# Performance work log

Hardware: AMD Instinct MI355X
Metric: run time of the kernel (lower is better)

Reference implementation:

```python
import jax, jax.numpy as jnp
import numpy as np
from jax import lax


def _cdist(a, b):
    # a: [B,N,D], b: [B,M,D] -> [B,N,M] euclidean distances (torch.cdist p=2)
    d2 = (jnp.sum(a * a, -1)[:, :, None]
          + jnp.sum(b * b, -1)[:, None, :]
          - 2.0 * jnp.einsum('bnd,bmd->bnm', a, b))
    return jnp.sqrt(jnp.maximum(d2, 0.0))


def _conv(x, w, b, pad):
    # x: [N,C,H,W], w: [O,I,kh,kw]
    y = lax.conv_general_dilated(x, w, (1, 1), [(pad, pad), (pad, pad)],
                                 dimension_numbers=('NCHW', 'OIHW', 'NCHW'))
    return y + b[None, :, None, None]


def setup_inputs() -> dict:
    key = jax.random.key(0)
    ks = jax.random.split(key, 10)
    Tq, Tk, D = 2048, 2048, 512
    return dict(
        seq_q=jax.random.normal(ks[0], (1, Tq, D), jnp.float32),
        seq_k=jax.random.normal(ks[1], (1, Tk, D), jnp.float32),
        len_q=jax.random.uniform(ks[2], (1, Tq), dtype=jnp.float32),
        len_k=jax.random.uniform(ks[3], (1, Tk), dtype=jnp.float32),
        conv1_w=jax.random.normal(ks[4], (30, 2, 5, 5), jnp.float32) * 0.1,
        conv1_b=jnp.zeros((30,), jnp.float32),
        conv2_w=jax.random.normal(ks[5], (30, 30, 5, 5), jnp.float32) * 0.05,
        conv2_b=jnp.zeros((30,), jnp.float32),
        conv3_w=jax.random.normal(ks[6], (1, 30, 3, 3), jnp.float32) * 0.1,
        conv3_b=jnp.zeros((1,), jnp.float32),
    )


def reference(seq_q, seq_k, len_q, len_k,
              conv1_w, conv1_b, conv2_w, conv2_b, conv3_w, conv3_b):
    B, Tq, _ = seq_q.shape
    Tk = seq_k.shape[1]
    D = _cdist(seq_q, seq_k)                          # [1,Tq,Tk]
    P = _cdist(len_q[..., None], len_k[..., None])    # [1,Tq,Tk]
    A = jnp.concatenate([D, P], 0)[None]              # [1,2,Tq,Tk]
    A = jax.nn.relu(_conv(A, conv1_w, conv1_b, 2))    # [1,30,Tq,Tk]
    A = jax.nn.relu(_conv(A, conv2_w, conv2_b, 2))    # [1,30,Tq,Tk]
    A = _conv(A, conv3_w, conv3_b, 1)[:, 0] + D       # [1,Tq,Tk] residual
    A = jax.nn.softmax(-A, axis=2)                    # row softmax
    At = A.reshape(B, Tq * Tk, 1)
    At = At / jnp.sum(jnp.abs(At), axis=1, keepdims=True)  # global L1 norm
    dis = jnp.matmul(D.reshape(B, 1, Tq * Tk), At)    # [1,1,1]
    return A, dis
```

## Files before the change

kernel.cpp:

```cpp
#include <hip/hip_runtime.h>

typedef short s8v __attribute__((ext_vector_type(8)));
typedef float f4v __attribute__((ext_vector_type(4)));

__device__ __forceinline__ unsigned short f2bf(float x) {
  union { float f; unsigned u; } v; v.f = x;
  unsigned r = v.u + 0x7fffu + ((v.u >> 16) & 1u);
  return (unsigned short)(r >> 16);
}
__device__ __forceinline__ unsigned pack_bf16x2(float lo, float hi) {
  unsigned r;
  asm("v_cvt_pk_bf16_f32 %0, %1, %2" : "=v"(r) : "v"(lo), "v"(hi));
  return r;
}
__device__ __forceinline__ s8v as_s8(int4 v) { union { int4 i; s8v s; } u; u.i = v; return u.s; }
__device__ __forceinline__ f4v as_f4(int4 v) { union { int4 i; f4v f; } u; u.i = v; return u.f; }
__device__ __forceinline__ int4 as_i4(f4v v) { union { f4v f; int4 i; } u; u.f = v; return u.i; }

__device__ __forceinline__ void bar_lgkm() {
  asm volatile("s_waitcnt lgkmcnt(0)" ::: "memory");
  __builtin_amdgcn_s_barrier();
  asm volatile("" ::: "memory");
}

__global__ __launch_bounds__(256) void prep_kernel(
    const float* __restrict__ q, const float* __restrict__ k,
    const float* __restrict__ w1, const float* __restrict__ w2, const float* __restrict__ w3,
    unsigned short* __restrict__ Qb, unsigned short* __restrict__ Kb,
    unsigned short* __restrict__ W1, unsigned short* __restrict__ W2,
    unsigned short* __restrict__ W3, float* __restrict__ nq, float* __restrict__ nk,
    float* __restrict__ accum) {
  int idx = blockIdx.x * 256 + threadIdx.x;
  const int NQ4 = (2048 * 512) / 4;
  if (idx < NQ4) {
    float4 v = ((const float4*)q)[idx];
    ((uint2*)Qb)[idx] = make_uint2(pack_bf16x2(v.x, v.y), pack_bf16x2(v.z, v.w));
    return;
  }
  idx -= NQ4;
  if (idx < NQ4) {
    float4 v = ((const float4*)k)[idx];
    ((uint2*)Kb)[idx] = make_uint2(pack_bf16x2(v.x, v.y), pack_bf16x2(v.z, v.w));
    return;
  }
  idx -= NQ4;
  if (idx < 4096 * 64) {
    int row = idx >> 6, l = idx & 63;
    const float* src = (row < 2048) ? (q + row * 512) : (k + (row - 2048) * 512);
    float s = 0.f;
#pragma unroll
    for (int i = 0; i < 8; ++i) { float v = src[l + i * 64]; s += v * v; }
    for (int off = 32; off; off >>= 1) s += __shfl_xor(s, off);
    if (l == 0) { if (row < 2048) nq[row] = s; else nk[row - 2048] = s; }
    return;
  }
  idx -= 4096 * 64;
  if (idx < 3072) {
    int j = idx >> 10, m = (idx >> 5) & 31, kk = idx & 31;
    int half = kk >> 4, kl = kk & 15, dy = 2 * j + half;
    float v = 0.f;
    if (m < 30 && kl < 10 && dy < 5) v = w1[m * 50 + (kl & 1) * 25 + dy * 5 + (kl >> 1)];
    W1[idx] = f2bf(v); return;
  }
  idx -= 3072;
  if (idx < 25600) {
    int dy = idx / 5120, r = idx - dy * 5120, m = r / 160, kk = r - m * 160;
    int c = kk & 31, dx = kk >> 5;
    float v = 0.f;
    if (m < 30 && c < 30) v = w2[m * 750 + c * 25 + dy * 5 + dx];
    W2[idx] = f2bf(v); return;
  }
  idx -= 25600;
  if (idx < 288) {
    int dd = idx >> 5, c = idx & 31;
    float v = (c < 30) ? w3[c * 9 + dd] : 0.f;
    W3[idx] = f2bf(v); return;
  }
  idx -= 288;
  if (idx == 0) *accum = 0.f;
}

__global__ __launch_bounds__(256) void dgemm_kernel(
    const unsigned short* __restrict__ Qb, const unsigned short* __restrict__ Kb,
    const float* __restrict__ nq, const float* __restrict__ nk,
    const float* __restrict__ lq, const float* __restrict__ lk,
    float* __restrict__ Dout, unsigned* __restrict__ DPo) {
  __shared__ int4 sm[2 * 128 * 9];
  const int t = threadIdx.x;
  const int bm = blockIdx.x, bn = blockIdx.y;
  const int wv = t >> 6, l = t & 63;
  const int m0 = (wv & 1) * 64, n0 = (wv >> 1) * 64;
  const int l15 = l & 15, q4 = l >> 4;
  f4v acc[4][4] = {};
  const int4* Qg = (const int4*)Qb;
  const int4* Kg = (const int4*)Kb;
  for (int kt = 0; kt < 8; ++kt) {
    __syncthreads();
#pragma unroll
    for (int i = 0; i < 4; ++i) {
      int c = t + i * 256;
      int row = c >> 3, kq = c & 7;
      sm[row * 9 + kq]        = Qg[(bm * 128 + row) * 64 + kt * 8 + kq];
      sm[1152 + row * 9 + kq] = Kg[(bn * 128 + row) * 64 + kt * 8 + kq];
    }
    __syncthreads();
#pragma unroll
    for (int s = 0; s < 2; ++s) {
      s8v af[4], bfr[4];
#pragma unroll
      for (int mt = 0; mt < 4; ++mt)
        af[mt] = as_s8(sm[(m0 + mt * 16 + l15) * 9 + s * 4 + q4]);
#pragma unroll
      for (int nt = 0; nt < 4; ++nt)
        bfr[nt] = as_s8(sm[1152 + (n0 + nt * 16 + l15) * 9 + s * 4 + q4]);
#pragma unroll
      for (int mt = 0; mt < 4; ++mt)
#pragma unroll
        for (int nt = 0; nt < 4; ++nt)
          acc[mt][nt] = __builtin_amdgcn_mfma_f32_16x16x32_bf16(af[mt], bfr[nt], acc[mt][nt], 0, 0, 0);
    }
  }
  float nkv[4], lkv[4];
#pragma unroll
  for (int nt = 0; nt < 4; ++nt) {
    int gc = bn * 128 + n0 + nt * 16 + l15;
    nkv[nt] = nk[gc]; lkv[nt] = lk[gc];
  }
#pragma unroll
  for (int mt = 0; mt < 4; ++mt)
#pragma unroll
    for (int reg = 0; reg < 4; ++reg) {
      int gr = bm * 128 + m0 + mt * 16 + q4 * 4 + reg;
      float nqv = nq[gr], lqv = lq[gr];
#pragma unroll
      for (int nt = 0; nt < 4; ++nt) {
        int gc = bn * 128 + n0 + nt * 16 + l15;
        float d2 = nqv + nkv[nt] - 2.f * acc[mt][nt][reg];
        float Dv = sqrtf(fmaxf(d2, 0.f));
        Dout[gr * 2048 + gc] = Dv;
        float Pv = fabsf(lqv - lkv[nt]);
        DPo[gr * 2048 + gc] = pack_bf16x2(Dv, Pv);
      }
    }
}

__global__ __launch_bounds__(512, 2) void fused_conv(
    const unsigned* __restrict__ DPg, const float* __restrict__ Dmat,
    const unsigned short* __restrict__ W1g, const unsigned short* __restrict__ W2g,
    const unsigned short* __restrict__ W3g,
    const float* __restrict__ b1, const float* __restrict__ b2, const float* __restrict__ b3,
    float* __restrict__ Sout) {
  __shared__ int4 a1s[1600];
  __shared__ int4 a2s[1360];
  __shared__ unsigned dps[1700];
  const int t = threadIdx.x;
  const int wv = t >> 6, l = t & 63, l15 = l & 15, q4 = l >> 4;
  const int x0 = blockIdx.x * 62, y0 = blockIdx.y * 32;

  int4 uni[25];
  int4 uni2[5];
  int4 ring2[5];
  float bias4[4];
  const int cls = (wv < 4) ? 0 : (wv < 6 ? 1 : 2);
  const int mb = (cls == 0) ? (wv >> 1) : (wv & 1);
  const int tp = (wv & 1) * 2;
  const int T3 = (wv - 6) * 2;

  unsigned pvO0 = 0u, pvO1 = 0u;
  float d0Oa = 0.f, d1Oa = 0.f, d0Ob = 0.f, d1Ob = 0.f;
  const int spx = (wv == 6) ? l : (64 + l);
  const int sgx = x0 - 5 + spx;
  const bool scol = (spx < 96) && (sgx >= 0) && (sgx < 2048);
  const int sgxc = min(max(sgx, 0), 2047);

  if (cls == 0) {
    const int4* W2i = (const int4*)W2g;
#pragma unroll
    for (int d = 0; d < 5; ++d)
#pragma unroll
      for (int s = 0; s < 5; ++s)
        uni[d * 5 + s] = W2i[(d * 32 + mb * 16 + l15) * 20 + s * 4 + q4];
#pragma unroll
    for (int j = 0; j < 5; ++j) { uni2[j] = make_int4(0, 0, 0, 0); ring2[j] = make_int4(0, 0, 0, 0); }
#pragma unroll
    for (int i = 0; i < 4; ++i) {
      int ch = mb * 16 + q4 * 4 + i;
      bias4[i] = (ch < 30) ? b2[ch] : 0.f;
    }
  } else if (cls == 1) {
    const int4* W1i = (const int4*)W1g;
#pragma unroll
    for (int j = 0; j < 3; ++j) uni2[j] = W1i[(j * 32 + mb * 16 + l15) * 4 + q4];
#pragma unroll
    for (int i = 0; i < 4; ++i) {
      int ch = mb * 16 + q4 * 4 + i;
      bias4[i] = (ch < 30) ? b1[ch] : 0.f;
    }
  } else {
    const int4* W3i = (const int4*)W3g;
#pragma unroll
    for (int dx = 0; dx < 3; ++dx)
      uni2[dx] = (l15 < 3) ? W3i[(l15 * 3 + dx) * 4 + q4] : make_int4(0, 0, 0, 0);
#pragma unroll
    for (int j = 0; j < 6; ++j) uni[j] = make_int4(0, 0, 0, 0);
    bias4[0] = b3[0];
    if (scol) {
      pvO0 = DPg[(y0 + 1) * 2048 + sgx];
      pvO1 = DPg[(y0 + 2) * 2048 + sgx];
    }
  }
  {
    int row = y0 - 5 + t / 96, px = t % 96;
    int gx = x0 - 5 + px;
    unsigned v = 0u;
    if (row >= 0 && gx >= 0 && gx < 2048) v = DPg[row * 2048 + gx];
    dps[(row & 15) * 100 + px] = v;
  }
  {
    int t2 = t + 512;
    if (t2 < 576) {
      int row = y0 - 5 + t2 / 96, px = t2 % 96;
      int gx = x0 - 5 + px;
      unsigned v = 0u;
      if (row >= 0 && gx >= 0 && gx < 2048) v = DPg[row * 2048 + gx];
      dps[(row & 15) * 100 + px] = v;
    }
  }
  if (t >= 144 && t < 224) {
    int i = t - 144;
    int sl = i >> 4, rem = i & 15;
    a2s[(sl * 68 + 64 + (rem >> 2)) * 4 + (rem & 3)] = make_int4(0, 0, 0, 0);
  }
  __syncthreads();

  for (int r = y0 - 3; r <= y0 + 37; r += 2) {
    if (cls == 0) {
#pragma unroll
      for (int sub = 0; sub < 2; ++sub) {
        int rc = r - 2 + sub;
        int s4 = rc & 3;
        int px0A = tp * 16 + l15;
        int px0B = px0A + 16;
        s8v fa = as_s8(a1s[(s4 * 80 + px0A) * 4 + (q4 ^ ((px0A >> 1) & 3))]);
        s8v fb = as_s8(a1s[(s4 * 80 + px0B) * 4 + (q4 ^ ((px0B >> 1) & 3))]);
        __builtin_amdgcn_s_setprio(1);
#pragma unroll
        for (int s = 0; s < 5; ++s) {
          s8v na = fa, nb = fb;
          if (s < 4) {
            int pxA = tp * 16 + l15 + s + 1;
            int pxB = pxA + 16;
            na = as_s8(a1s[(s4 * 80 + pxA) * 4 + (q4 ^ ((pxA >> 1) & 3))]);
            nb = as_s8(a1s[(s4 * 80 + pxB) * 4 + (q4 ^ ((pxB >> 1) & 3))]);
          }
#pragma unroll
          for (int d = 4; d >= 0; --d)
            uni2[4 - d] = as_i4(__builtin_amdgcn_mfma_f32_16x16x32_bf16(
                as_s8(uni[d * 5 + s]), fa, as_f4(uni2[4 - d]), 0, 0, 0));
#pragma unroll
          for (int d = 4; d >= 0; --d)
            ring2[4 - d] = as_i4(__builtin_amdgcn_mfma_f32_16x16x32_bf16(
                as_s8(uni[d * 5 + s]), fb, as_f4(ring2[4 - d]), 0, 0, 0));
          fa = na; fb = nb;
        }
        __builtin_amdgcn_s_setprio(0);
        int r2c = rc - 2;
        bool vrow = (r2c >= y0 - 1 && r2c <= y0 + 32);
        int slotrow = vrow ? (r2c & 3) : 4;
        bool rowin = vrow && (r2c >= 0) && (r2c < 2048);
        {
          int px2 = tp * 16 + l15;
          int gx2 = x0 - 1 + px2;
          bool ok = rowin && (gx2 >= 0) && (gx2 < 2048);
          f4v a = as_f4(uni2[0]);
          float v0 = ok ? fmaxf(a[0] + bias4[0], 0.f) : 0.f;
          float v1 = ok ? fmaxf(a[1] + bias4[1], 0.f) : 0.f;
          float v2 = ok ? fmaxf(a[2] + bias4[2], 0.f) : 0.f;
          float v3 = ok ? fmaxf(a[3] + bias4[3], 0.f) : 0.f;
          int slot = (mb * 2 + (q4 >> 1)) ^ ((px2 >> 1) & 3);
          *(uint2*)((unsigned short*)a2s + (slotrow * 68 + px2) * 32 + slot * 8 + (q4 & 1) * 4) =
              make_uint2(pack_bf16x2(v0, v1), pack_bf16x2(v2, v3));
        }
        {
          int px2 = tp * 16 + 16 + l15;
          int gx2 = x0 - 1 + px2;
          bool ok = rowin && (gx2 >= 0) && (gx2 < 2048);
          f4v a = as_f4(ring2[0]);
          float v0 = ok ? fmaxf(a[0] + bias4[0], 0.f) : 0.f;
          float v1 = ok ? fmaxf(a[1] + bias4[1], 0.f) : 0.f;
          float v2 = ok ? fmaxf(a[2] + bias4[2], 0.f) : 0.f;
          float v3 = ok ? fmaxf(a[3] + bias4[3], 0.f) : 0.f;
          int slot = (mb * 2 + (q4 >> 1)) ^ ((px2 >> 1) & 3);
          *(uint2*)((unsigned short*)a2s + (slotrow * 68 + px2) * 32 + slot * 8 + (q4 & 1) * 4) =
              make_uint2(pack_bf16x2(v0, v1), pack_bf16x2(v2, v3));
        }
#pragma unroll
        for (int j = 0; j < 4; ++j) { uni2[j] = uni2[j + 1]; ring2[j] = ring2[j + 1]; }
        uni2[4] = make_int4(0, 0, 0, 0);
        ring2[4] = make_int4(0, 0, 0, 0);
      }
    } else if (cls == 1) {
#pragma unroll
      for (int pr = 0; pr < 2; ++pr) {
        int p = r + pr;
        f4v a5[5];
        int4 c0, c1, c2;
        {
          int px = l15;
          int rl0 = p - 2, rl1 = p, rl2 = p + 2;
          int rs0 = (q4 < 2) ? rl0 : (rl0 + 1);
          int rs1 = (q4 < 2) ? rl1 : (rl1 + 1);
          c0 = *(const int4*)(dps + (rs0 & 15) * 100 + px + (q4 & 1) * 4);
          c1 = *(const int4*)(dps + (rs1 & 15) * 100 + px + (q4 & 1) * 4);
          c2 = *(const int4*)(dps + (rl2 & 15) * 100 + px + (q4 & 1) * 4);
        }
        __builtin_amdgcn_s_setprio(1);
#pragma unroll
        for (int T1 = 0; T1 < 5; ++T1) {
          int4 n0 = c0, n1 = c1, n2 = c2;
          if (T1 < 4) {
            int px = (T1 + 1) * 16 + l15;
            int rl0 = p - 2, rl1 = p, rl2 = p + 2;
            int rs0 = (q4 < 2) ? rl0 : (rl0 + 1);
            int rs1 = (q4 < 2) ? rl1 : (rl1 + 1);
            n0 = *(const int4*)(dps + (rs0 & 15) * 100 + px + (q4 & 1) * 4);
            n1 = *(const int4*)(dps + (rs1 & 15) * 100 + px + (q4 & 1) * 4);
            n2 = *(const int4*)(dps + (rl2 & 15) * 100 + px + (q4 & 1) * 4);
          }
          f4v acc = {0.f, 0.f, 0.f, 0.f};
          acc = __builtin_amdgcn_mfma_f32_16x16x32_bf16(as_s8(uni2[0]), as_s8(c0), acc, 0, 0, 0);
          acc = __builtin_amdgcn_mfma_f32_16x16x32_bf16(as_s8(uni2[1]), as_s8(c1), acc, 0, 0, 0);
          acc = __builtin_amdgcn_mfma_f32_16x16x32_bf16(as_s8(uni2[2]), as_s8(c2), acc, 0, 0, 0);
          a5[T1] = acc;
          c0 = n0; c1 = n1; c2 = n2;
        }
        __builtin_amdgcn_s_setprio(0);
        bool vrow = (p >= y0 - 3 && p <= y0 + 34);
        int slotrow = vrow ? (p & 3) : 4;
        bool rowok = vrow && (p >= 0 && p < 2048);
#pragma unroll
        for (int T1 = 0; T1 < 5; ++T1) {
          int px = T1 * 16 + l15;
          int gx = x0 - 3 + px;
          bool ok = rowok && gx >= 0 && gx < 2048;
          float v0 = ok ? fmaxf(a5[T1][0] + bias4[0], 0.f) : 0.f;
          float v1 = ok ? fmaxf(a5[T1][1] + bias4[1], 0.f) : 0.f;
          float v2 = ok ? fmaxf(a5[T1][2] + bias4[2], 0.f) : 0.f;
          float v3 = ok ? fmaxf(a5[T1][3] + bias4[3], 0.f) : 0.f;
          int slot = (mb * 2 + (q4 >> 1)) ^ ((px >> 1) & 3);
          *(uint2*)((unsigned short*)a1s + (slotrow * 80 + px) * 32 + slot * 8 + (q4 & 1) * 4) =
              make_uint2(pack_bf16x2(v0, v1), pack_bf16x2(v2, v3));
        }
      }
    } else {
      int rsN0 = r + 6, rsN1 = r + 7;
      unsigned tmp0 = DPg[min(rsN0, 2047) * 2048 + sgxc];
      unsigned tmp1 = DPg[min(rsN1, 2047) * 2048 + sgxc];
      unsigned pvN0 = (scol && rsN0 < 2048) ? tmp0 : 0u;
      unsigned pvN1 = (scol && rsN1 < 2048) ? tmp1 : 0u;
      int gx0 = x0 + T3 * 16 + l15;
      int gx0c = min(gx0, 2047), gx1c = min(gx0 + 16, 2047);
      int yn0c = min(max(r - 5, 0), 2047), yn1c = min(max(r - 4, 0), 2047);
      float d0Na = Dmat[yn0c * 2048 + gx0c];
      float d1Na = Dmat[yn0c * 2048 + gx1c];
      float d0Nb = Dmat[yn1c * 2048 + gx0c];
      float d1Nb = Dmat[yn1c * 2048 + gx1c];
      s8v Bf[12];
#pragma unroll
      for (int sub = 0; sub < 2; ++sub) {
        int s4 = (r - 6 + sub) & 3;
#pragma unroll
        for (int tt = 0; tt < 2; ++tt)
#pragma unroll
          for (int dx = 0; dx < 3; ++dx) {
            int px2 = (T3 + tt) * 16 + l15 + dx;
            Bf[sub * 6 + tt * 3 + dx] =
                as_s8(a2s[(s4 * 68 + px2) * 4 + (q4 ^ ((px2 >> 1) & 3))]);
          }
      }
      float eA0, eA1, eA2, eA3, eA4, eA5;
      {
        __builtin_amdgcn_s_setprio(1);
#pragma unroll
        for (int tt = 0; tt < 2; ++tt) {
          f4v acc3 = {0.f, 0.f, 0.f, 0.f};
#pragma unroll
          for (int dx = 0; dx < 3; ++dx)
            acc3 = __builtin_amdgcn_mfma_f32_16x16x32_bf16(
                as_s8(uni2[dx]), Bf[tt * 3 + dx], acc3, 0, 0, 0);
          uni[tt * 3 + 2] = as_i4(acc3);
        }
        __builtin_amdgcn_s_setprio(0);
        eA0 = as_f4(uni[0])[0]; eA1 = as_f4(uni[1])[1]; eA2 = as_f4(uni[2])[2];
        eA3 = as_f4(uni[3])[0]; eA4 = as_f4(uni[4])[1]; eA5 = as_f4(uni[5])[2];
#pragma unroll
        for (int tt = 0; tt < 2; ++tt) {
          uni[tt * 3 + 0] = uni[tt * 3 + 1];
          uni[tt * 3 + 1] = uni[tt * 3 + 2];
        }
      }
      float eB0, eB1, eB2, eB3, eB4, eB5;
      {
        __builtin_amdgcn_s_setprio(1);
#pragma unroll
        for (int tt = 0; tt < 2; ++tt) {
          f4v acc3 = {0.f, 0.f, 0.f, 0.f};
#pragma unroll
          for (int dx = 0; dx < 3; ++dx)
            acc3 = __builtin_amdgcn_mfma_f32_16x16x32_bf16(
                as_s8(uni2[dx]), Bf[6 + tt * 3 + dx], acc3, 0, 0, 0);
          uni[tt * 3 + 2] = as_i4(acc3);
        }
        __builtin_amdgcn_s_setprio(0);
        eB0 = as_f4(uni[0])[0]; eB1 = as_f4(uni[1])[1]; eB2 = as_f4(uni[2])[2];
        eB3 = as_f4(uni[3])[0]; eB4 = as_f4(uni[4])[1]; eB5 = as_f4(uni[5])[2];
#pragma unroll
        for (int tt = 0; tt < 2; ++tt) {
          uni[tt * 3 + 0] = uni[tt * 3 + 1];
          uni[tt * 3 + 1] = uni[tt * 3 + 2];
        }
      }
      {
        int y = r - 7;
        bool yok = (y >= y0 && y <= y0 + 31);
        int gxa = x0 + T3 * 16 + l15;
        int gxb = gxa + 16;
        if (q4 == 0 && yok && gxa < 2048)
          Sout[y * 2048 + gxa] = eA0 + eA1 + eA2 + bias4[0] + d0Oa;
        if (q4 == 0 && yok && (T3 + 1) * 16 + l15 < 62 && gxb < 2048)
          Sout[y * 2048 + gxb] = eA3 + eA4 + eA5 + bias4[0] + d1Oa;
      }
      {
        int y = r - 6;
        bool yok = (y >= y0 && y <= y0 + 31);
        int gxa = x0 + T3 * 16 + l15;
        int gxb = gxa + 16;
        if (q4 == 0 && yok && gxa < 2048)
          Sout[y * 2048 + gxa] = eB0 + eB1 + eB2 + bias4[0] + d0Ob;
        if (q4 == 0 && yok && (T3 + 1) * 16 + l15 < 62 && gxb < 2048)
          Sout[y * 2048 + gxb] = eB3 + eB4 + eB5 + bias4[0] + d1Ob;
      }
      {
        int rs0 = r + 4, rs1 = r + 5;
        int wr0 = (rs0 <= y0 + 36) ? (rs0 & 15) : 16;
        int wr1 = (rs1 <= y0 + 36) ? (rs1 & 15) : 16;
        if (spx < 96) {
          dps[wr0 * 100 + spx] = pvO0;
          dps[wr1 * 100 + spx] = pvO1;
        }
      }
      pvO0 = pvN0; pvO1 = pvN1;
      d0Oa = d0Na; d1Oa = d1Na; d0Ob = d0Nb; d1Ob = d1Nb;
    }
    bar_lgkm();
  }
}

__global__ __launch_bounds__(256) void softmax_kernel(
    float* __restrict__ S, const float* __restrict__ Dmat, float* __restrict__ accum) {
  const int row = blockIdx.x, t = threadIdx.x;
  float* Srow = S + row * 2048;
  const float* Drow = Dmat + row * 2048;
  float sv[8], dv[8];
  float mx = -1e30f;
#pragma unroll
  for (int i = 0; i < 8; ++i) {
    sv[i] = -Srow[t + i * 256];
    dv[i] = Drow[t + i * 256];
    mx = fmaxf(mx, sv[i]);
  }
  __shared__ float red[4], redz[4], redw[4];
  for (int off = 32; off; off >>= 1) mx = fmaxf(mx, __shfl_xor(mx, off));
  const int wv = t >> 6, l = t & 63;
  if (l == 0) red[wv] = mx;
  __syncthreads();
  mx = fmaxf(fmaxf(red[0], red[1]), fmaxf(red[2], red[3]));
  float z = 0.f, w = 0.f, ev[8];
#pragma unroll
  for (int i = 0; i < 8; ++i) {
    ev[i] = __expf(sv[i] - mx);
    z += ev[i];
    w += ev[i] * dv[i];
  }
  for (int off = 32; off; off >>= 1) { z += __shfl_xor(z, off); w += __shfl_xor(w, off); }
  if (l == 0) { redz[wv] = z; redw[wv] = w; }
  __syncthreads();
  z = redz[0] + redz[1] + redz[2] + redz[3];
  w = redw[0] + redw[1] + redw[2] + redw[3];
  float inv = 1.f / z;
#pragma unroll
  for (int i = 0; i < 8; ++i) Srow[t + i * 256] = ev[i] * inv;
  if (t == 0) atomicAdd(accum, w * inv);
}

__global__ void finalize_kernel(const float* __restrict__ accum, float* __restrict__ out) {
  if (threadIdx.x == 0) out[0] = accum[0] * (1.f / 2048.f);
}

extern "C" void kernel_launch(void* const* d_in, const int* in_sizes, int n_in,
                              void* d_out, int out_size, void* d_ws, size_t ws_size,
                              hipStream_t stream) {
  const float* seq_q = (const float*)d_in[0];
  const float* seq_k = (const float*)d_in[1];
  const float* len_q = (const float*)d_in[2];
  const float* len_k = (const float*)d_in[3];
  const float* w1 = (const float*)d_in[4];
  const float* b1 = (const float*)d_in[5];
  const float* w2 = (const float*)d_in[6];
  const float* b2 = (const float*)d_in[7];
  const float* w3 = (const float*)d_in[8];
  const float* b3 = (const float*)d_in[9];

  char* ws = (char*)d_ws;
  unsigned short* Qb  = (unsigned short*)(ws);
  unsigned short* Kb  = (unsigned short*)(ws + ((size_t)2 << 20));
  float* nq           = (float*)(ws + ((size_t)4 << 20));
  float* nk           = (float*)(ws + ((size_t)4 << 20) + 16384);
  unsigned short* W1  = (unsigned short*)(ws + ((size_t)4 << 20) + 32768);
  unsigned short* W2  = (unsigned short*)(ws + ((size_t)4 << 20) + 65536);
  unsigned short* W3  = (unsigned short*)(ws + ((size_t)4 << 20) + 131072);
  float* accum        = (float*)(ws + ((size_t)4 << 20) + 163840);
  float* Dmat         = (float*)(ws + ((size_t)5 << 20));
  unsigned* DPo       = (unsigned*)(ws + ((size_t)22 << 20));
  float* out = (float*)d_out;

  const int prep_total = 2 * ((2048 * 512) / 4) + 4096 * 64 + 3072 + 25600 + 288 + 1;
  prep_kernel<<<(prep_total + 255) / 256, 256, 0, stream>>>(
      seq_q, seq_k, w1, w2, w3, Qb, Kb, W1, W2, W3, nq, nk, accum);
  dgemm_kernel<<<dim3(16, 16), 256, 0, stream>>>(Qb, Kb, nq, nk, len_q, len_k, Dmat, DPo);
  fused_conv<<<dim3(34, 64), 512, 0, stream>>>(
      DPo, Dmat, W1, W2, W3, b1, b2, b3, out);
  softmax_kernel<<<2048, 256, 0, stream>>>(out, Dmat, accum);
  finalize_kernel<<<1, 64, 0, stream>>>(accum, out + 4194304);
}
```

Baseline: 486.1 us.

## Spread conv2 work across all eight waves and give each wave a secondary role

```diff
diff --git a/kernel.cpp b/kernel.cpp
--- a/kernel.cpp
+++ b/kernel.cpp
@@ -158,56 +158,58 @@
   const int x0 = blockIdx.x * 62, y0 = blockIdx.y * 32;
 
   int4 uni[25];
-  int4 uni2[5];
-  int4 ring2[5];
-  float bias4[4];
-  const int cls = (wv < 4) ? 0 : (wv < 6 ? 1 : 2);
-  const int mb = (cls == 0) ? (wv >> 1) : (wv & 1);
-  const int tp = (wv & 1) * 2;
-  const int T3 = (wv - 6) * 2;
-
-  unsigned pvO0 = 0u, pvO1 = 0u;
-  float d0Oa = 0.f, d1Oa = 0.f, d0Ob = 0.f, d1Ob = 0.f;
-  const int spx = (wv == 6) ? l : (64 + l);
+  int4 ring[5];
+  int4 sec[3];
+  int4 cs[6];
+  float bias2[4];
+  float biasS[4];
+  const int mbA = wv >> 2;
+  const int tp1 = wv & 3;
+  const int role = (wv < 2) ? 1 : (wv < 4 ? 2 : 3);
+  const int mbB = wv & 1;
+  const int T3 = (wv - 2) * 2;
+  const int srow = (wv >= 6) ? 1 : 0;
+  const int spx = (wv & 1) * 64 + l;
   const int sgx = x0 - 5 + spx;
   const bool scol = (spx < 96) && (sgx >= 0) && (sgx < 2048);
   const int sgxc = min(max(sgx, 0), 2047);
-
-  if (cls == 0) {
+  unsigned pvO = 0u;
+  float d0Oa = 0.f, d1Oa = 0.f, d0Ob = 0.f, d1Ob = 0.f;
+
+  {
     const int4* W2i = (const int4*)W2g;
 #pragma unroll
     for (int d = 0; d < 5; ++d)
 #pragma unroll
       for (int s = 0; s < 5; ++s)
-        uni[d * 5 + s] = W2i[(d * 32 + mb * 16 + l15) * 20 + s * 4 + q4];
-#pragma unroll
-    for (int j = 0; j < 5; ++j) { uni2[j] = make_int4(0, 0, 0, 0); ring2[j] = make_int4(0, 0, 0, 0); }
+        uni[d * 5 + s] = W2i[(d * 32 + mbA * 16 + l15) * 20 + s * 4 + q4];
+#pragma unroll
+    for (int j = 0; j < 5; ++j) ring[j] = make_int4(0, 0, 0, 0);
 #pragma unroll
     for (int i = 0; i < 4; ++i) {
-      int ch = mb * 16 + q4 * 4 + i;
-      bias4[i] = (ch < 30) ? b2[ch] : 0.f;
-    }
-  } else if (cls == 1) {
+      int ch = mbA * 16 + q4 * 4 + i;
+      bias2[i] = (ch < 30) ? b2[ch] : 0.f;
+    }
+  }
+  if (role == 1) {
     const int4* W1i = (const int4*)W1g;
 #pragma unroll
-    for (int j = 0; j < 3; ++j) uni2[j] = W1i[(j * 32 + mb * 16 + l15) * 4 + q4];
+    for (int j = 0; j < 3; ++j) sec[j] = W1i[(j * 32 + mbB * 16 + l15) * 4 + q4];
 #pragma unroll
     for (int i = 0; i < 4; ++i) {
-      int ch = mb * 16 + q4 * 4 + i;
-      bias4[i] = (ch < 30) ? b1[ch] : 0.f;
-    }
+      int ch = mbB * 16 + q4 * 4 + i;
+      biasS[i] = (ch < 30) ? b1[ch] : 0.f;
+    }
+  } else if (role == 2) {
+    const int4* W3i = (const int4*)W3g;
+#pragma unroll
+    for (int dx = 0; dx < 3; ++dx)
+      sec[dx] = (l15 < 3) ? W3i[(l15 * 3 + dx) * 4 + q4] : make_int4(0, 0, 0, 0);
+#pragma unroll
+    for (int j = 0; j < 6; ++j) cs[j] = make_int4(0, 0, 0, 0);
+    biasS[0] = b3[0];
   } else {
-    const int4* W3i = (const int4*)W3g;
-#pragma unroll
-    for (int dx = 0; dx < 3; ++dx)
-      uni2[dx] = (l15 < 3) ? W3i[(l15 * 3 + dx) * 4 + q4] : make_int4(0, 0, 0, 0);
-#pragma unroll
-    for (int j = 0; j < 6; ++j) uni[j] = make_int4(0, 0, 0, 0);
-    bias4[0] = b3[0];
-    if (scol) {
-      pvO0 = DPg[(y0 + 1) * 2048 + sgx];
-      pvO1 = DPg[(y0 + 2) * 2048 + sgx];
-    }
+    if (scol) pvO = DPg[(y0 + 1 + srow) * 2048 + sgx];
   }
   {
     int row = y0 - 5 + t / 96, px = t % 96;
@@ -234,72 +236,90 @@
   __syncthreads();
 
   for (int r = y0 - 3; r <= y0 + 37; r += 2) {
-    if (cls == 0) {
-#pragma unroll
-      for (int sub = 0; sub < 2; ++sub) {
-        int rc = r - 2 + sub;
-        int s4 = rc & 3;
-        int px0A = tp * 16 + l15;
-        int px0B = px0A + 16;
-        s8v fa = as_s8(a1s[(s4 * 80 + px0A) * 4 + (q4 ^ ((px0A >> 1) & 3))]);
-        s8v fb = as_s8(a1s[(s4 * 80 + px0B) * 4 + (q4 ^ ((px0B >> 1) & 3))]);
-        __builtin_amdgcn_s_setprio(1);
-#pragma unroll
-        for (int s = 0; s < 5; ++s) {
-          s8v na = fa, nb = fb;
-          if (s < 4) {
-            int pxA = tp * 16 + l15 + s + 1;
-            int pxB = pxA + 16;
-            na = as_s8(a1s[(s4 * 80 + pxA) * 4 + (q4 ^ ((pxA >> 1) & 3))]);
-            nb = as_s8(a1s[(s4 * 80 + pxB) * 4 + (q4 ^ ((pxB >> 1) & 3))]);
-          }
-#pragma unroll
-          for (int d = 4; d >= 0; --d)
-            uni2[4 - d] = as_i4(__builtin_amdgcn_mfma_f32_16x16x32_bf16(
-                as_s8(uni[d * 5 + s]), fa, as_f4(uni2[4 - d]), 0, 0, 0));
-#pragma unroll
-          for (int d = 4; d >= 0; --d)
-            ring2[4 - d] = as_i4(__builtin_amdgcn_mfma_f32_16x16x32_bf16(
-                as_s8(uni[d * 5 + s]), fb, as_f4(ring2[4 - d]), 0, 0, 0));
-          fa = na; fb = nb;
-        }
-        __builtin_amdgcn_s_setprio(0);
-        int r2c = rc - 2;
-        bool vrow = (r2c >= y0 - 1 && r2c <= y0 + 32);
-        int slotrow = vrow ? (r2c & 3) : 4;
-        bool rowin = vrow && (r2c >= 0) && (r2c < 2048);
-        {
-          int px2 = tp * 16 + l15;
-          int gx2 = x0 - 1 + px2;
-          bool ok = rowin && (gx2 >= 0) && (gx2 < 2048);
-          f4v a = as_f4(uni2[0]);
-          float v0 = ok ? fmaxf(a[0] + bias4[0], 0.f) : 0.f;
-          float v1 = ok ? fmaxf(a[1] + bias4[1], 0.f) : 0.f;
-          float v2 = ok ? fmaxf(a[2] + bias4[2], 0.f) : 0.f;
-          float v3 = ok ? fmaxf(a[3] + bias4[3], 0.f) : 0.f;
-          int slot = (mb * 2 + (q4 >> 1)) ^ ((px2 >> 1) & 3);
-          *(uint2*)((unsigned short*)a2s + (slotrow * 68 + px2) * 32 + slot * 8 + (q4 & 1) * 4) =
-              make_uint2(pack_bf16x2(v0, v1), pack_bf16x2(v2, v3));
-        }
-        {
-          int px2 = tp * 16 + 16 + l15;
-          int gx2 = x0 - 1 + px2;
-          bool ok = rowin && (gx2 >= 0) && (gx2 < 2048);
-          f4v a = as_f4(ring2[0]);
-          float v0 = ok ? fmaxf(a[0] + bias4[0], 0.f) : 0.f;
-          float v1 = ok ? fmaxf(a[1] + bias4[1], 0.f) : 0.f;
-          float v2 = ok ? fmaxf(a[2] + bias4[2], 0.f) : 0.f;
-          float v3 = ok ? fmaxf(a[3] + bias4[3], 0.f) : 0.f;
-          int slot = (mb * 2 + (q4 >> 1)) ^ ((px2 >> 1) & 3);
-          *(uint2*)((unsigned short*)a2s + (slotrow * 68 + px2) * 32 + slot * 8 + (q4 & 1) * 4) =
-              make_uint2(pack_bf16x2(v0, v1), pack_bf16x2(v2, v3));
-        }
-#pragma unroll
-        for (int j = 0; j < 4; ++j) { uni2[j] = uni2[j + 1]; ring2[j] = ring2[j + 1]; }
-        uni2[4] = make_int4(0, 0, 0, 0);
-        ring2[4] = make_int4(0, 0, 0, 0);
-      }
-    } else if (cls == 1) {
+    unsigned pvN = 0u;
+    float d0Na = 0.f, d1Na = 0.f, d0Nb = 0.f, d1Nb = 0.f;
+    if (role == 3) {
+      int rsN = r + 6 + srow;
+      unsigned tmp = DPg[min(rsN, 2047) * 2048 + sgxc];
+      pvN = (scol && rsN < 2048) ? tmp : 0u;
+    } else if (role == 2) {
+      int gx0 = x0 + T3 * 16 + l15;
+      int gx0c = min(gx0, 2047), gx1c = min(gx0 + 16, 2047);
+      int yn0c = min(max(r - 5, 0), 2047), yn1c = min(max(r - 4, 0), 2047);
+      d0Na = Dmat[yn0c * 2048 + gx0c];
+      d1Na = Dmat[yn0c * 2048 + gx1c];
+      d0Nb = Dmat[yn1c * 2048 + gx0c];
+      d1Nb = Dmat[yn1c * 2048 + gx1c];
+    }
+
+    int4 pA, pB;
+    {
+      int s4 = (r - 2) & 3;
+      int px0 = tp1 * 16 + l15;
+      s8v fa = as_s8(a1s[(s4 * 80 + px0) * 4 + (q4 ^ ((px0 >> 1) & 3))]);
+      __builtin_amdgcn_s_setprio(1);
+#pragma unroll
+      for (int s = 0; s < 5; ++s) {
+        s8v na = fa;
+        if (s < 4) {
+          int px = tp1 * 16 + l15 + s + 1;
+          na = as_s8(a1s[(s4 * 80 + px) * 4 + (q4 ^ ((px >> 1) & 3))]);
+        }
+#pragma unroll
+        for (int d = 4; d >= 0; --d)
+          ring[4 - d] = as_i4(__builtin_amdgcn_mfma_f32_16x16x32_bf16(
+              as_s8(uni[d * 5 + s]), fa, as_f4(ring[4 - d]), 0, 0, 0));
+        fa = na;
+      }
+      __builtin_amdgcn_s_setprio(0);
+      pA = ring[0];
+#pragma unroll
+      for (int j = 0; j < 4; ++j) ring[j] = ring[j + 1];
+      ring[4] = make_int4(0, 0, 0, 0);
+    }
+    {
+      int s4 = (r - 1) & 3;
+      int px0 = tp1 * 16 + l15;
+      s8v fa = as_s8(a1s[(s4 * 80 + px0) * 4 + (q4 ^ ((px0 >> 1) & 3))]);
+      __builtin_amdgcn_s_setprio(1);
+#pragma unroll
+      for (int s = 0; s < 5; ++s) {
+        s8v na = fa;
+        if (s < 4) {
+          int px = tp1 * 16 + l15 + s + 1;
+          na = as_s8(a1s[(s4 * 80 + px) * 4 + (q4 ^ ((px >> 1) & 3))]);
+        }
+#pragma unroll
+        for (int d = 4; d >= 0; --d)
+          ring[4 - d] = as_i4(__builtin_amdgcn_mfma_f32_16x16x32_bf16(
+              as_s8(uni[d * 5 + s]), fa, as_f4(ring[4 - d]), 0, 0, 0));
+        fa = na;
+      }
+      __builtin_amdgcn_s_setprio(0);
+      pB = ring[0];
+#pragma unroll
+      for (int j = 0; j < 4; ++j) ring[j] = ring[j + 1];
+      ring[4] = make_int4(0, 0, 0, 0);
+    }
+#pragma unroll
+    for (int e = 0; e < 2; ++e) {
+      int r2c = r - 4 + e;
+      f4v a = as_f4(e ? pB : pA);
+      bool vrow = (r2c >= y0 - 1 && r2c <= y0 + 32);
+      int slotrow = vrow ? (r2c & 3) : 4;
+      int px2 = tp1 * 16 + l15;
+      int gx2 = x0 - 1 + px2;
+      bool ok = vrow && (r2c >= 0) && (r2c < 2048) && (gx2 >= 0) && (gx2 < 2048);
+      float v0 = ok ? fmaxf(a[0] + bias2[0], 0.f) : 0.f;
+      float v1 = ok ? fmaxf(a[1] + bias2[1], 0.f) : 0.f;
+      float v2 = ok ? fmaxf(a[2] + bias2[2], 0.f) : 0.f;
+      float v3 = ok ? fmaxf(a[3] + bias2[3], 0.f) : 0.f;
+      int slot = (mbA * 2 + (q4 >> 1)) ^ ((px2 >> 1) & 3);
+      *(uint2*)((unsigned short*)a2s + (slotrow * 68 + px2) * 32 + slot * 8 + (q4 & 1) * 4) =
+          make_uint2(pack_bf16x2(v0, v1), pack_bf16x2(v2, v3));
+    }
+
+    if (role == 1) {
 #pragma unroll
       for (int pr = 0; pr < 2; ++pr) {
         int p = r + pr;
@@ -328,9 +348,9 @@
             n2 = *(const int4*)(dps + (rl2 & 15) * 100 + px + (q4 & 1) * 4);
           }
           f4v acc = {0.f, 0.f, 0.f, 0.f};
-          acc = __builtin_amdgcn_mfma_f32_16x16x32_bf16(as_s8(uni2[0]), as_s8(c0), acc, 0, 0, 0);
-          acc = __builtin_amdgcn_mfma_f32_16x16x32_bf16(as_s8(uni2[1]), as_s8(c1), acc, 0, 0, 0);
-          acc = __builtin_amdgcn_mfma_f32_16x16x32_bf16(as_s8(uni2[2]), as_s8(c2), acc, 0, 0, 0);
+          acc = __builtin_amdgcn_mfma_f32_16x16x32_bf16(as_s8(sec[0]), as_s8(c0), acc, 0, 0, 0);
+          acc = __builtin_amdgcn_mfma_f32_16x16x32_bf16(as_s8(sec[1]), as_s8(c1), acc, 0, 0, 0);
+          acc = __builtin_amdgcn_mfma_f32_16x16x32_bf16(as_s8(sec[2]), as_s8(c2), acc, 0, 0, 0);
           a5[T1] = acc;
           c0 = n0; c1 = n1; c2 = n2;
         }
@@ -343,43 +363,27 @@
           int px = T1 * 16 + l15;
           int gx = x0 - 3 + px;
           bool ok = rowok && gx >= 0 && gx < 2048;
-          float v0 = ok ? fmaxf(a5[T1][0] + bias4[0], 0.f) : 0.f;
-          float v1 = ok ? fmaxf(a5[T1][1] + bias4[1], 0.f) : 0.f;
-          float v2 = ok ? fmaxf(a5[T1][2] + bias4[2], 0.f) : 0.f;
-          float v3 = ok ? fmaxf(a5[T1][3] + bias4[3], 0.f) : 0.f;
-          int slot = (mb * 2 + (q4 >> 1)) ^ ((px >> 1) & 3);
+          float v0 = ok ? fmaxf(a5[T1][0] + biasS[0], 0.f) : 0.f;
+          float v1 = ok ? fmaxf(a5[T1][1] + biasS[1], 0.f) : 0.f;
+          float v2 = ok ? fmaxf(a5[T1][2] + biasS[2], 0.f) : 0.f;
+          float v3 = ok ? fmaxf(a5[T1][3] + biasS[3], 0.f) : 0.f;
+          int slot = (mbB * 2 + (q4 >> 1)) ^ ((px >> 1) & 3);
           *(uint2*)((unsigned short*)a1s + (slotrow * 80 + px) * 32 + slot * 8 + (q4 & 1) * 4) =
               make_uint2(pack_bf16x2(v0, v1), pack_bf16x2(v2, v3));
         }
       }
-    } else {
-      int rsN0 = r + 6, rsN1 = r + 7;
-      unsigned tmp0 = DPg[min(rsN0, 2047) * 2048 + sgxc];
-      unsigned tmp1 = DPg[min(rsN1, 2047) * 2048 + sgxc];
-      unsigned pvN0 = (scol && rsN0 < 2048) ? tmp0 : 0u;
-      unsigned pvN1 = (scol && rsN1 < 2048) ? tmp1 : 0u;
-      int gx0 = x0 + T3 * 16 + l15;
-      int gx0c = min(gx0, 2047), gx1c = min(gx0 + 16, 2047);
-      int yn0c = min(max(r - 5, 0), 2047), yn1c = min(max(r - 4, 0), 2047);
-      float d0Na = Dmat[yn0c * 2048 + gx0c];
-      float d1Na = Dmat[yn0c * 2048 + gx1c];
-      float d0Nb = Dmat[yn1c * 2048 + gx0c];
-      float d1Nb = Dmat[yn1c * 2048 + gx1c];
-      s8v Bf[12];
-#pragma unroll
-      for (int sub = 0; sub < 2; ++sub) {
-        int s4 = (r - 6 + sub) & 3;
+    } else if (role == 2) {
+      float eA0, eA1, eA2, eA3, eA4, eA5;
+      {
+        int s4 = (r - 6) & 3;
+        s8v Bf[6];
 #pragma unroll
         for (int tt = 0; tt < 2; ++tt)
 #pragma unroll
           for (int dx = 0; dx < 3; ++dx) {
             int px2 = (T3 + tt) * 16 + l15 + dx;
-            Bf[sub * 6 + tt * 3 + dx] =
-                as_s8(a2s[(s4 * 68 + px2) * 4 + (q4 ^ ((px2 >> 1) & 3))]);
+            Bf[tt * 3 + dx] = as_s8(a2s[(s4 * 68 + px2) * 4 + (q4 ^ ((px2 >> 1) & 3))]);
           }
-      }
-      float eA0, eA1, eA2, eA3, eA4, eA5;
-      {
         __builtin_amdgcn_s_setprio(1);
 #pragma unroll
         for (int tt = 0; tt < 2; ++tt) {
@@ -387,20 +391,29 @@
 #pragma unroll
           for (int dx = 0; dx < 3; ++dx)
             acc3 = __builtin_amdgcn_mfma_f32_16x16x32_bf16(
-                as_s8(uni2[dx]), Bf[tt * 3 + dx], acc3, 0, 0, 0);
-          uni[tt * 3 + 2] = as_i4(acc3);
+                as_s8(sec[dx]), Bf[tt * 3 + dx], acc3, 0, 0, 0);
+          cs[tt * 3 + 2] = as_i4(acc3);
         }
         __builtin_amdgcn_s_setprio(0);
-        eA0 = as_f4(uni[0])[0]; eA1 = as_f4(uni[1])[1]; eA2 = as_f4(uni[2])[2];
-        eA3 = as_f4(uni[3])[0]; eA4 = as_f4(uni[4])[1]; eA5 = as_f4(uni[5])[2];
+        eA0 = as_f4(cs[0])[0]; eA1 = as_f4(cs[1])[1]; eA2 = as_f4(cs[2])[2];
+        eA3 = as_f4(cs[3])[0]; eA4 = as_f4(cs[4])[1]; eA5 = as_f4(cs[5])[2];
 #pragma unroll
         for (int tt = 0; tt < 2; ++tt) {
-          uni[tt * 3 + 0] = uni[tt * 3 + 1];
-          uni[tt * 3 + 1] = uni[tt * 3 + 2];
+          cs[tt * 3 + 0] = cs[tt * 3 + 1];
+          cs[tt * 3 + 1] = cs[tt * 3 + 2];
         }
       }
       float eB0, eB1, eB2, eB3, eB4, eB5;
       {
+        int s4 = (r - 5) & 3;
+        s8v Bf[6];
+#pragma unroll
+        for (int tt = 0; tt < 2; ++tt)
+#pragma unroll
+          for (int dx = 0; dx < 3; ++dx) {
+            int px2 = (T3 + tt) * 16 + l15 + dx;
+            Bf[tt * 3 + dx] = as_s8(a2s[(s4 * 68 + px2) * 4 + (q4 ^ ((px2 >> 1) & 3))]);
+          }
         __builtin_amdgcn_s_setprio(1);
 #pragma unroll
         for (int tt = 0; tt < 2; ++tt) {
@@ -408,16 +421,16 @@
 #pragma unroll
           for (int dx = 0; dx < 3; ++dx)
             acc3 = __builtin_amdgcn_mfma_f32_16x16x32_bf16(
-                as_s8(uni2[dx]), Bf[6 + tt * 3 + dx], acc3, 0, 0, 0);
-          uni[tt * 3 + 2] = as_i4(acc3);
+                as_s8(sec[dx]), Bf[tt * 3 + dx], acc3, 0, 0, 0);
+          cs[tt * 3 + 2] = as_i4(acc3);
         }
         __builtin_amdgcn_s_setprio(0);
-        eB0 = as_f4(uni[0])[0]; eB1 = as_f4(uni[1])[1]; eB2 = as_f4(uni[2])[2];
-        eB3 = as_f4(uni[3])[0]; eB4 = as_f4(uni[4])[1]; eB5 = as_f4(uni[5])[2];
+        eB0 = as_f4(cs[0])[0]; eB1 = as_f4(cs[1])[1]; eB2 = as_f4(cs[2])[2];
+        eB3 = as_f4(cs[3])[0]; eB4 = as_f4(cs[4])[1]; eB5 = as_f4(cs[5])[2];
 #pragma unroll
         for (int tt = 0; tt < 2; ++tt) {
-          uni[tt * 3 + 0] = uni[tt * 3 + 1];
-          uni[tt * 3 + 1] = uni[tt * 3 + 2];
+          cs[tt * 3 + 0] = cs[tt * 3 + 1];
+          cs[tt * 3 + 1] = cs[tt * 3 + 2];
         }
       }
       {
@@ -426,9 +439,9 @@
         int gxa = x0 + T3 * 16 + l15;
         int gxb = gxa + 16;
         if (q4 == 0 && yok && gxa < 2048)
-          Sout[y * 2048 + gxa] = eA0 + eA1 + eA2 + bias4[0] + d0Oa;
+          Sout[y * 2048 + gxa] = eA0 + eA1 + eA2 + biasS[0] + d0Oa;
         if (q4 == 0 && yok && (T3 + 1) * 16 + l15 < 62 && gxb < 2048)
-          Sout[y * 2048 + gxb] = eA3 + eA4 + eA5 + bias4[0] + d1Oa;
+          Sout[y * 2048 + gxb] = eA3 + eA4 + eA5 + biasS[0] + d1Oa;
       }
       {
         int y = r - 6;
@@ -436,21 +449,16 @@
         int gxa = x0 + T3 * 16 + l15;
         int gxb = gxa + 16;
         if (q4 == 0 && yok && gxa < 2048)
-          Sout[y * 2048 + gxa] = eB0 + eB1 + eB2 + bias4[0] + d0Ob;
+          Sout[y * 2048 + gxa] = eB0 + eB1 + eB2 + biasS[0] + d0Ob;
         if (q4 == 0 && yok && (T3 + 1) * 16 + l15 < 62 && gxb < 2048)
-          Sout[y * 2048 + gxb] = eB3 + eB4 + eB5 + bias4[0] + d1Ob;
-      }
-      {
-        int rs0 = r + 4, rs1 = r + 5;
-        int wr0 = (rs0 <= y0 + 36) ? (rs0 & 15) : 16;
-        int wr1 = (rs1 <= y0 + 36) ? (rs1 & 15) : 16;
-        if (spx < 96) {
-          dps[wr0 * 100 + spx] = pvO0;
-          dps[wr1 * 100 + spx] = pvO1;
-        }
-      }
-      pvO0 = pvN0; pvO1 = pvN1;
+          Sout[y * 2048 + gxb] = eB3 + eB4 + eB5 + biasS[0] + d1Ob;
+      }
       d0Oa = d0Na; d1Oa = d1Na; d0Ob = d0Nb; d1Ob = d1Nb;
+    } else {
+      int rs = r + 4 + srow;
+      int wr = (rs <= y0 + 36) ? (rs & 15) : 16;
+      if (spx < 96) dps[wr * 100 + spx] = pvO;
+      pvO = pvN;
     }
     bar_lgkm();
   }
```

Measured after the change: 519.9 us. 1.07x slower.

## Taller conv row tiles, fuse row norms into bf16 cast, lighter GEMM barriers

Applied to the files above, without the earlier changes.

```diff
diff --git a/kernel.cpp b/kernel.cpp
--- a/kernel.cpp
+++ b/kernel.cpp
@@ -30,31 +30,33 @@
     unsigned short* __restrict__ W1, unsigned short* __restrict__ W2,
     unsigned short* __restrict__ W3, float* __restrict__ nq, float* __restrict__ nk,
     float* __restrict__ accum) {
+  __shared__ float part[4];
   int idx = blockIdx.x * 256 + threadIdx.x;
   const int NQ4 = (2048 * 512) / 4;
-  if (idx < NQ4) {
-    float4 v = ((const float4*)q)[idx];
-    ((uint2*)Qb)[idx] = make_uint2(pack_bf16x2(v.x, v.y), pack_bf16x2(v.z, v.w));
+  if (idx < 2 * NQ4) {
+    const bool isK = (idx >= NQ4);
+    int ci = isK ? (idx - NQ4) : idx;
+    float4 v = isK ? ((const float4*)k)[ci] : ((const float4*)q)[ci];
+    uint2 pk = make_uint2(pack_bf16x2(v.x, v.y), pack_bf16x2(v.z, v.w));
+    if (isK) ((uint2*)Kb)[ci] = pk; else ((uint2*)Qb)[ci] = pk;
+    float s = v.x * v.x + v.y * v.y + v.z * v.z + v.w * v.w;
+    for (int off = 32; off; off >>= 1) s += __shfl_xor(s, off);
+    int wid = threadIdx.x >> 6;
+    if ((threadIdx.x & 63) == 0) part[wid] = s;
+    __syncthreads();
+    if (threadIdx.x == 0) {
+      int row = ci >> 7;
+      float t = part[0] + part[1];
+      if (isK) nk[row] = t; else nq[row] = t;
+    }
+    if (threadIdx.x == 128) {
+      int row = ci >> 7;
+      float t = part[2] + part[3];
+      if (isK) nk[row] = t; else nq[row] = t;
+    }
     return;
   }
-  idx -= NQ4;
-  if (idx < NQ4) {
-    float4 v = ((const float4*)k)[idx];
-    ((uint2*)Kb)[idx] = make_uint2(pack_bf16x2(v.x, v.y), pack_bf16x2(v.z, v.w));
-    return;
-  }
-  idx -= NQ4;
-  if (idx < 4096 * 64) {
-    int row = idx >> 6, l = idx & 63;
-    const float* src = (row < 2048) ? (q + row * 512) : (k + (row - 2048) * 512);
-    float s = 0.f;
-#pragma unroll
-    for (int i = 0; i < 8; ++i) { float v = src[l + i * 64]; s += v * v; }
-    for (int off = 32; off; off >>= 1) s += __shfl_xor(s, off);
-    if (l == 0) { if (row < 2048) nq[row] = s; else nk[row - 2048] = s; }
-    return;
-  }
-  idx -= 4096 * 64;
+  idx -= 2 * NQ4;
   if (idx < 3072) {
     int j = idx >> 10, m = (idx >> 5) & 31, kk = idx & 31;
     int half = kk >> 4, kl = kk & 15, dy = 2 * j + half;
@@ -95,7 +97,7 @@
   const int4* Qg = (const int4*)Qb;
   const int4* Kg = (const int4*)Kb;
   for (int kt = 0; kt < 8; ++kt) {
-    __syncthreads();
+    bar_lgkm();
 #pragma unroll
     for (int i = 0; i < 4; ++i) {
       int c = t + i * 256;
@@ -103,7 +105,7 @@
       sm[row * 9 + kq]        = Qg[(bm * 128 + row) * 64 + kt * 8 + kq];
       sm[1152 + row * 9 + kq] = Kg[(bn * 128 + row) * 64 + kt * 8 + kq];
     }
-    __syncthreads();
+    bar_lgkm();
 #pragma unroll
     for (int s = 0; s < 2; ++s) {
       s8v af[4], bfr[4];
@@ -155,7 +157,7 @@
   __shared__ unsigned dps[1700];
   const int t = threadIdx.x;
   const int wv = t >> 6, l = t & 63, l15 = l & 15, q4 = l >> 4;
-  const int x0 = blockIdx.x * 62, y0 = blockIdx.y * 32;
+  const int x0 = blockIdx.x * 62, y0 = blockIdx.y * 48;
 
   int4 uni[25];
   int4 uni2[5];
@@ -233,7 +235,7 @@
   }
   __syncthreads();
 
-  for (int r = y0 - 3; r <= y0 + 37; r += 2) {
+  for (int r = y0 - 3; r <= y0 + 53; r += 2) {
     if (cls == 0) {
 #pragma unroll
       for (int sub = 0; sub < 2; ++sub) {
@@ -265,7 +267,7 @@
         }
         __builtin_amdgcn_s_setprio(0);
         int r2c = rc - 2;
-        bool vrow = (r2c >= y0 - 1 && r2c <= y0 + 32);
+        bool vrow = (r2c >= y0 - 1 && r2c <= y0 + 48);
         int slotrow = vrow ? (r2c & 3) : 4;
         bool rowin = vrow && (r2c >= 0) && (r2c < 2048);
         {
@@ -335,7 +337,7 @@
           c0 = n0; c1 = n1; c2 = n2;
         }
         __builtin_amdgcn_s_setprio(0);
-        bool vrow = (p >= y0 - 3 && p <= y0 + 34);
+        bool vrow = (p >= y0 - 3 && p <= y0 + 50);
         int slotrow = vrow ? (p & 3) : 4;
         bool rowok = vrow && (p >= 0 && p < 2048);
 #pragma unroll
@@ -422,7 +424,7 @@
       }
       {
         int y = r - 7;
-        bool yok = (y >= y0 && y <= y0 + 31);
+        bool yok = (y >= y0 && y <= y0 + 47 && y < 2048);
         int gxa = x0 + T3 * 16 + l15;
         int gxb = gxa + 16;
         if (q4 == 0 && yok && gxa < 2048)
@@ -432,7 +434,7 @@
       }
       {
         int y = r - 6;
-        bool yok = (y >= y0 && y <= y0 + 31);
+        bool yok = (y >= y0 && y <= y0 + 47 && y < 2048);
         int gxa = x0 + T3 * 16 + l15;
         int gxb = gxa + 16;
         if (q4 == 0 && yok && gxa < 2048)
@@ -442,8 +444,8 @@
       }
       {
         int rs0 = r + 4, rs1 = r + 5;
-        int wr0 = (rs0 <= y0 + 36) ? (rs0 & 15) : 16;
-        int wr1 = (rs1 <= y0 + 36) ? (rs1 & 15) : 16;
+        int wr0 = (rs0 <= y0 + 52) ? (rs0 & 15) : 16;
+        int wr1 = (rs1 <= y0 + 52) ? (rs1 & 15) : 16;
         if (spx < 96) {
           dps[wr0 * 100 + spx] = pvO0;
           dps[wr1 * 100 + spx] = pvO1;
@@ -524,11 +526,11 @@
   unsigned* DPo       = (unsigned*)(ws + ((size_t)22 << 20));
   float* out = (float*)d_out;
 
-  const int prep_total = 2 * ((2048 * 512) / 4) + 4096 * 64 + 3072 + 25600 + 288 + 1;
+  const int prep_total = 2 * ((2048 * 512) / 4) + 3072 + 25600 + 288 + 1;
   prep_kernel<<<(prep_total + 255) / 256, 256, 0, stream>>>(
       seq_q, seq_k, w1, w2, w3, Qb, Kb, W1, W2, W3, nq, nk, accum);
   dgemm_kernel<<<dim3(16, 16), 256, 0, stream>>>(Qb, Kb, nq, nk, len_q, len_k, Dmat, DPo);
-  fused_conv<<<dim3(34, 64), 512, 0, stream>>>(
+  fused_conv<<<dim3(34, 43), 512, 0, stream>>>(
       DPo, Dmat, W1, W2, W3, b1, b2, b3, out);
   softmax_kernel<<<2048, 256, 0, stream>>>(out, Dmat, accum);
   finalize_kernel<<<1, 64, 0, stream>>>(accum, out + 4194304);
```

Result: faster. 447.6 us (-7.9%).
